# Kernel tuning notes

Measured on AMD Instinct MI355X. Metric: run time of the kernel, lower is better.

The kernel has to match this reference:

```python
import jax, jax.numpy as jnp
import numpy as np

DIM = 1024
DEPTH = 4
HEADS = 16
MLP_DIM = 4096
EPS = 1e-5


def layer_norm(x, g, b):
    mu = jnp.mean(x, axis=-1, keepdims=True)
    var = jnp.mean(jnp.square(x - mu), axis=-1, keepdims=True)
    return (x - mu) * jax.lax.rsqrt(var + EPS) * g + b


def setup_inputs() -> dict:
    key = jax.random.key(0)
    ks = jax.random.split(key, 8)
    s = DIM ** -0.5
    return {
        "x": jax.random.normal(ks[0], (2, 1024, DIM), dtype=jnp.float32),
        "ln1_g": jnp.ones((DIM,), jnp.float32),
        "ln1_b": jnp.zeros((DIM,), jnp.float32),
        "w_qkv": jax.random.normal(ks[1], (DIM, 3 * DIM), jnp.float32) * s,
        "w_o": jax.random.normal(ks[2], (DIM, DIM), jnp.float32) * s,
        "b_o": jnp.zeros((DIM,), jnp.float32),
        "ln2_g": jnp.ones((DIM,), jnp.float32),
        "ln2_b": jnp.zeros((DIM,), jnp.float32),
        "w1": jax.random.normal(ks[3], (DIM, MLP_DIM), jnp.float32) * s,
        "b1": jnp.zeros((MLP_DIM,), jnp.float32),
        "w2": jax.random.normal(ks[4], (MLP_DIM, DIM), jnp.float32) * (MLP_DIM ** -0.5),
        "b2": jnp.zeros((DIM,), jnp.float32),
    }


def reference(x, ln1_g, ln1_b, w_qkv, w_o, b_o, ln2_g, ln2_b, w1, b1, w2, b2):
    b, n, _ = x.shape
    h, d = HEADS, DIM // HEADS
    scale = DIM ** -0.5  # NB: full dim, as in source
    for _ in range(DEPTH):  # same (shared) weights each layer, per ModuleList([m]*depth)
        # --- attention with pre-norm + residual ---
        xn = layer_norm(x, ln1_g, ln1_b)
        qkv = xn @ w_qkv  # [b, n, 3*dim]
        qkv = qkv.reshape(b, n, 3, h, d)
        q = qkv[:, :, 0].transpose(0, 2, 1, 3)  # [b, h, n, d]
        k = qkv[:, :, 1].transpose(0, 2, 1, 3)
        v = qkv[:, :, 2].transpose(0, 2, 1, 3)
        scores = jnp.einsum('bhid,bhjd->bhij', q, k) * scale
        attn = jax.nn.softmax(scores, axis=-1)
        out = jnp.einsum('bhij,bhjd->bhid', attn, v)
        out = out.transpose(0, 2, 1, 3).reshape(b, n, DIM)
        x = out @ w_o + b_o + x
        # --- MLP with pre-norm + residual ---
        xn = layer_norm(x, ln2_g, ln2_b)
        hdn = jax.nn.gelu(xn @ w1 + b1, approximate=False)
        x = hdn @ w2 + b2 + x
    return x
```

## Files before the change

kernel.cpp:

```cpp
#include <hip/hip_runtime.h>
#include <math.h>

#define NTOK 2048
#define DIM_ 1024
#define NSEQ 1024
#define HEADS_ 16
#define HD 64
#define MLP_ 4096
#define EPS_ 1e-5f

#define FLAG_BIAS  1
#define FLAG_GELU  2
#define FLAG_QKV   8
#define FLAG_PART  16

typedef __attribute__((ext_vector_type(8))) short bf16x8;
typedef __attribute__((ext_vector_type(4))) float f32x4;

__device__ __forceinline__ unsigned short f2bf(float f) {
    unsigned u = __float_as_uint(f);
    u += 0x7fffu + ((u >> 16) & 1u);
    return (unsigned short)(u >> 16);
}
__device__ __forceinline__ float bf2f(unsigned short u) {
    return __uint_as_float(((unsigned)u) << 16);
}
__device__ __forceinline__ void gld16(const unsigned short* g, short* l) {
    __builtin_amdgcn_global_load_lds(
        (const __attribute__((address_space(1))) void*)g,
        (__attribute__((address_space(3))) void*)l, 16, 0, 0);
}
__device__ __forceinline__ float gelu_fast(float v) {
    float u = 1.5957691f * (v + 0.044715f * v * v * v);
    return v / (1.0f + __expf(-u));
}

__global__ __launch_bounds__(256) void wconv_kernel(const float* __restrict__ W,
                                                    unsigned short* __restrict__ Wt,
                                                    int K, int N,
                                                    float qscale, int qcols) {
    __shared__ float s[32][33];
    int n0 = blockIdx.x * 32, k0 = blockIdx.y * 32;
    int tx = threadIdx.x, ty = threadIdx.y;
    #pragma unroll
    for (int r = 0; r < 4; r++) {
        int k = ty + r * 8;
        s[k][tx] = W[(size_t)(k0 + k) * N + n0 + tx];
    }
    __syncthreads();
    #pragma unroll
    for (int r = 0; r < 4; r++) {
        int n = ty + r * 8;
        float v = s[tx][n];
        if (n0 + n < qcols) v *= qscale;
        Wt[(size_t)(n0 + n) * K + k0 + tx] = f2bf(v);
    }
}

__global__ __launch_bounds__(256) void ln_kernel(const float* __restrict__ src,
                                                 unsigned short* __restrict__ dst,
                                                 const float* __restrict__ g,
                                                 const float* __restrict__ b) {
    int row = blockIdx.x;
    int t = threadIdx.x;
    const float4* x4 = (const float4*)(src + (size_t)row * DIM_);
    float4 f = x4[t];
    float s  = f.x + f.y + f.z + f.w;
    float sq = f.x*f.x + f.y*f.y + f.z*f.z + f.w*f.w;
    __shared__ float ssum[256], ssq[256];
    ssum[t] = s; ssq[t] = sq;
    __syncthreads();
    for (int o = 128; o > 0; o >>= 1) {
        if (t < o) { ssum[t] += ssum[t+o]; ssq[t] += ssq[t+o]; }
        __syncthreads();
    }
    float mu  = ssum[0] * (1.0f / DIM_);
    float var = ssq[0] * (1.0f / DIM_) - mu * mu;
    float r = rsqrtf(var + EPS_);
    const float4* g4 = (const float4*)g;
    const float4* b4 = (const float4*)b;
    float4 gg = g4[t], bb = b4[t];
    ushort4 o4;
    o4.x = f2bf((f.x - mu) * r * gg.x + bb.x);
    o4.y = f2bf((f.y - mu) * r * gg.y + bb.y);
    o4.z = f2bf((f.z - mu) * r * gg.z + bb.z);
    o4.w = f2bf((f.w - mu) * r * gg.w + bb.w);
    ((ushort4*)(dst + (size_t)row * DIM_))[t] = o4;
}

__global__ __launch_bounds__(256) void gemm128_kernel(const unsigned short* __restrict__ A,
                                                      const unsigned short* __restrict__ Bt,
                                                      unsigned short* __restrict__ Cb,
                                                      unsigned short* __restrict__ Vt,
                                                      unsigned short* __restrict__ Ppart,
                                                      const float* __restrict__ bias,
                                                      int M, int N, int K, int KC,
                                                      int ldcb, int nx, int gz, int flags) {
    __shared__ short As[128 * 64];
    __shared__ short Bs[128 * 64];
    int id = blockIdx.x;
    int xcd = id & 7, s = id >> 3;
    int x = s % nx, pl = s / nx;
    int pair = pl * 8 + xcd;
    int z = pair % gz, y = pair / gz;
    int col0 = x * 128, row0 = y * 128;
    int k_beg = z * KC, k_end = k_beg + KC;

    int t = threadIdx.x;
    int lane = t & 63, w = t >> 6;
    int wm = w & 1, wn = w >> 1;

    f32x4 acc[4][4];
    #pragma unroll
    for (int mi = 0; mi < 4; mi++)
        #pragma unroll
        for (int ni = 0; ni < 4; ni++) acc[mi][ni] = (f32x4){0.f, 0.f, 0.f, 0.f};

    int r0 = t >> 3;
    int lchunk = ((t & 7) ^ (r0 & 7)) * 8;
    const unsigned short* Ag = A  + (size_t)(row0 + r0) * K + lchunk;
    const unsigned short* Bg = Bt + (size_t)(col0 + r0) * K + lchunk;
    short* Al = As + t * 8;
    short* Bl = Bs + t * 8;

    int m_l = lane & 15, quad = lane >> 4;
    int sw7 = m_l & 7;

    for (int k0 = k_beg; k0 < k_end; k0 += 64) {
        #pragma unroll
        for (int i = 0; i < 4; i++) {
            gld16(Ag + k0 + (size_t)i * 32 * K, Al + i * 2048);
            gld16(Bg + k0 + (size_t)i * 32 * K, Bl + i * 2048);
        }
        __syncthreads();

        #pragma unroll
        for (int kf = 0; kf < 2; kf++) {
            int cb = ((kf * 4 + quad) ^ sw7) * 8;
            bf16x8 af[4], bfr[4];
            #pragma unroll
            for (int mi = 0; mi < 4; mi++)
                af[mi]  = *(const bf16x8*)&As[(wm * 64 + mi * 16 + m_l) * 64 + cb];
            #pragma unroll
            for (int ni = 0; ni < 4; ni++)
                bfr[ni] = *(const bf16x8*)&Bs[(wn * 64 + ni * 16 + m_l) * 64 + cb];
            #pragma unroll
            for (int mi = 0; mi < 4; mi++)
                #pragma unroll
                for (int ni = 0; ni < 4; ni++)
                    acc[mi][ni] = __builtin_amdgcn_mfma_f32_16x16x32_bf16(af[mi], bfr[ni],
                                                                          acc[mi][ni], 0, 0, 0);
        }
        __syncthreads();
    }

    if (flags & FLAG_PART) {
        unsigned short* P = Ppart + (size_t)z * M * N;
        #pragma unroll
        for (int mi = 0; mi < 4; mi++)
            #pragma unroll
            for (int ni = 0; ni < 4; ni++) {
                int col = col0 + wn * 64 + ni * 16 + m_l;
                #pragma unroll
                for (int r = 0; r < 4; r++) {
                    int row = row0 + wm * 64 + mi * 16 + quad * 4 + r;
                    P[(size_t)row * N + col] = f2bf(acc[mi][ni][r]);
                }
            }
        return;
    }

    int colw = col0 + wn * 64;
    if ((flags & FLAG_QKV) && colw >= 2048) {
        int h = (colw - 2048) >> 6;
        #pragma unroll
        for (int mi = 0; mi < 4; mi++) {
            int tok0 = row0 + wm * 64 + mi * 16 + quad * 4;
            int bb = tok0 >> 10, nn = tok0 & 1023;
            #pragma unroll
            for (int ni = 0; ni < 4; ni++) {
                int d = ni * 16 + m_l;
                ushort4 o4;
                o4.x = f2bf(acc[mi][ni][0]);
                o4.y = f2bf(acc[mi][ni][1]);
                o4.z = f2bf(acc[mi][ni][2]);
                o4.w = f2bf(acc[mi][ni][3]);
                *(ushort4*)(Vt + ((size_t)(bb * 16 + h) * 64 + d) * 1024 + nn) = o4;
            }
        }
        return;
    }

    #pragma unroll
    for (int mi = 0; mi < 4; mi++)
        #pragma unroll
        for (int ni = 0; ni < 4; ni++) {
            int col = colw + ni * 16 + m_l;
            float bv = (flags & FLAG_BIAS) ? bias[col] : 0.0f;
            #pragma unroll
            for (int r = 0; r < 4; r++) {
                int row = row0 + wm * 64 + mi * 16 + quad * 4 + r;
                float v = acc[mi][ni][r] + bv;
                if (flags & FLAG_GELU) v = gelu_fast(v);
                Cb[(size_t)row * ldcb + col] = f2bf(v);
            }
        }
}

__global__ __launch_bounds__(256) void reduce_ln_kernel(const unsigned short* __restrict__ P,
                                                        int nsplit,
                                                        const float* __restrict__ bias,
                                                        const float* __restrict__ resid,
                                                        float* __restrict__ xc_out,
                                                        unsigned short* __restrict__ xn_out,
                                                        const float* __restrict__ g,
                                                        const float* __restrict__ b) {
    const int MN = NTOK * DIM_;
    int row = blockIdx.x;
    int t = threadIdx.x;
    size_t i = (size_t)row * DIM_ + t * 4;
    float4 y  = *(const float4*)(resid + i);
    float4 bi = *(const float4*)(bias + t * 4);
    y.x += bi.x; y.y += bi.y; y.z += bi.z; y.w += bi.w;
    for (int z = 0; z < nsplit; z++) {
        ushort4 p = *(const ushort4*)(P + (size_t)z * MN + i);
        y.x += bf2f(p.x); y.y += bf2f(p.y); y.z += bf2f(p.z); y.w += bf2f(p.w);
    }
    *(float4*)(xc_out + i) = y;
    if (!xn_out) return;

    float s  = y.x + y.y + y.z + y.w;
    float sq = y.x*y.x + y.y*y.y + y.z*y.z + y.w*y.w;
    __shared__ float ssum[256], ssq[256];
    ssum[t] = s; ssq[t] = sq;
    __syncthreads();
    for (int o = 128; o > 0; o >>= 1) {
        if (t < o) { ssum[t] += ssum[t+o]; ssq[t] += ssq[t+o]; }
        __syncthreads();
    }
    float mu  = ssum[0] * (1.0f / DIM_);
    float var = ssq[0] * (1.0f / DIM_) - mu * mu;
    float r = rsqrtf(var + EPS_);
    float4 gg = *(const float4*)(g + t * 4);
    float4 bb = *(const float4*)(b + t * 4);
    ushort4 o4;
    o4.x = f2bf((y.x - mu) * r * gg.x + bb.x);
    o4.y = f2bf((y.y - mu) * r * gg.y + bb.y);
    o4.z = f2bf((y.z - mu) * r * gg.z + bb.z);
    o4.w = f2bf((y.w - mu) * r * gg.w + bb.w);
    ((ushort4*)(xn_out + (size_t)row * DIM_))[t] = o4;
}

__global__ __launch_bounds__(512) void fattn_kernel(const unsigned short* __restrict__ qk,
                                                    const unsigned short* __restrict__ VtG,
                                                    unsigned short* __restrict__ out) {
    int idx = blockIdx.x;
    int qt = idx & 7;
    int h  = (idx >> 3) & 15;
    int b  = idx >> 7;
    int t  = threadIdx.x;
    int lane = t & 63, w = t >> 6;
    int m = lane & 15, quad = lane >> 4;

    __shared__ unsigned short Ks[64 * 64];
    __shared__ unsigned short Vs[64 * 64];
    __shared__ unsigned short Ps[8][16 * 72];

    const size_t base = (size_t)b * NSEQ * 2048;
    const int i0 = qt * 128 + w * 16;

    bf16x8 aq0, aq1;
    {
        const unsigned short* qrow = qk + base + (size_t)(i0 + m) * 2048 + h * HD;
        aq0 = *(const bf16x8*)(qrow + quad * 8);
        aq1 = *(const bf16x8*)(qrow + 32 + quad * 8);
    }

    f32x4 Oacc[4];
    #pragma unroll
    for (int dt = 0; dt < 4; dt++) Oacc[dt] = (f32x4){0.f, 0.f, 0.f, 0.f};
    float lsum[4] = {0.f, 0.f, 0.f, 0.f};

    int srow = t >> 3;
    int schunk = t & 7;
    int swc = schunk ^ (srow & 7);
    const unsigned short* Kg = qk + base + 1024 + h * HD + (size_t)srow * 2048 + schunk * 8;
    const unsigned short* Vg = VtG + ((size_t)(b * 16 + h) * 64 + srow) * 1024 + schunk * 8;
    unsigned short* Kl = &Ks[srow * 64 + swc * 8];
    unsigned short* Vl = &Vs[srow * 64 + swc * 8];

    for (int j0 = 0; j0 < NSEQ; j0 += 64) {
        *(bf16x8*)Kl = *(const bf16x8*)(Kg + (size_t)j0 * 2048);
        *(bf16x8*)Vl = *(const bf16x8*)(Vg + j0);
        __syncthreads();

        f32x4 s[4];
        #pragma unroll
        for (int nt = 0; nt < 4; nt++) {
            int jr = nt * 16 + m;
            const unsigned short* kr = &Ks[jr * 64];
            int x7 = jr & 7;
            bf16x8 b0 = *(const bf16x8*)(kr + (quad ^ x7) * 8);
            bf16x8 b1 = *(const bf16x8*)(kr + ((quad + 4) ^ x7) * 8);
            f32x4 a = (f32x4){0.f, 0.f, 0.f, 0.f};
            a = __builtin_amdgcn_mfma_f32_16x16x32_bf16(aq0, b0, a, 0, 0, 0);
            a = __builtin_amdgcn_mfma_f32_16x16x32_bf16(aq1, b1, a, 0, 0, 0);
            s[nt] = a;
        }

        #pragma unroll
        for (int r = 0; r < 4; r++) {
            float p0 = __expf(s[0][r]);
            float p1 = __expf(s[1][r]);
            float p2 = __expf(s[2][r]);
            float p3 = __expf(s[3][r]);
            lsum[r] += p0 + p1 + p2 + p3;
            unsigned short* pr = &Ps[w][(quad * 4 + r) * 72 + m];
            pr[0]  = f2bf(p0);
            pr[16] = f2bf(p1);
            pr[32] = f2bf(p2);
            pr[48] = f2bf(p3);
        }

        const unsigned short* pa = &Ps[w][m * 72 + quad * 8];
        bf16x8 ap0 = *(const bf16x8*)pa;
        bf16x8 ap1 = *(const bf16x8*)(pa + 32);
        #pragma unroll
        for (int dt = 0; dt < 4; dt++) {
            int dr = dt * 16 + m;
            const unsigned short* vr = &Vs[dr * 64];
            int x7 = dr & 7;
            bf16x8 b0 = *(const bf16x8*)(vr + (quad ^ x7) * 8);
            bf16x8 b1 = *(const bf16x8*)(vr + ((quad + 4) ^ x7) * 8);
            Oacc[dt] = __builtin_amdgcn_mfma_f32_16x16x32_bf16(ap0, b0, Oacc[dt], 0, 0, 0);
            Oacc[dt] = __builtin_amdgcn_mfma_f32_16x16x32_bf16(ap1, b1, Oacc[dt], 0, 0, 0);
        }
        __syncthreads();
    }

    #pragma unroll
    for (int r = 0; r < 4; r++) {
        float rs = lsum[r];
        rs += __shfl_xor(rs, 1);
        rs += __shfl_xor(rs, 2);
        rs += __shfl_xor(rs, 4);
        rs += __shfl_xor(rs, 8);
        lsum[r] = rs;
    }

    #pragma unroll
    for (int r = 0; r < 4; r++) {
        float inv = 1.0f / lsum[r];
        int row = i0 + quad * 4 + r;
        unsigned short* orow = out + ((size_t)(b * NSEQ + row)) * DIM_ + h * HD + m;
        orow[0]  = f2bf(Oacc[0][r] * inv);
        orow[16] = f2bf(Oacc[1][r] * inv);
        orow[32] = f2bf(Oacc[2][r] * inv);
        orow[48] = f2bf(Oacc[3][r] * inv);
    }
}

extern "C" void kernel_launch(void* const* d_in, const int* in_sizes, int n_in,
                              void* d_out, int out_size, void* d_ws, size_t ws_size,
                              hipStream_t stream) {
    const float* x    = (const float*)d_in[0];
    const float* ln1g = (const float*)d_in[1];
    const float* ln1b = (const float*)d_in[2];
    const float* wqkv = (const float*)d_in[3];
    const float* wo   = (const float*)d_in[4];
    const float* bo   = (const float*)d_in[5];
    const float* ln2g = (const float*)d_in[6];
    const float* ln2b = (const float*)d_in[7];
    const float* w1   = (const float*)d_in[8];
    const float* b1   = (const float*)d_in[9];
    const float* w2   = (const float*)d_in[10];
    const float* b2   = (const float*)d_in[11];
    float* out = (float*)d_out;

    char* ws = (char*)d_ws;
    float*          xcur = (float*)(ws);
    unsigned short* aout = (unsigned short*)(ws + (8u<<20));
    unsigned short* xn   = (unsigned short*)(ws + (12u<<20));
    unsigned short* qk   = (unsigned short*)(ws + (16u<<20));
    unsigned short* VtG  = (unsigned short*)(ws + (24u<<20));
    unsigned short* hdn  = (unsigned short*)(ws + (28u<<20));
    unsigned short* wtqkv= (unsigned short*)(ws + (44u<<20));
    unsigned short* wto  = (unsigned short*)(ws + (50u<<20));
    unsigned short* wt1  = (unsigned short*)(ws + (52u<<20));
    unsigned short* wt2  = (unsigned short*)(ws + (60u<<20));
    unsigned short* opart  = (unsigned short*)(ws + (12u<<20));
    unsigned short* m2part = (unsigned short*)(ws + (8u<<20));

    wconv_kernel<<<dim3(3*DIM_/32, DIM_/32), dim3(32,8), 0, stream>>>(wqkv, wtqkv, DIM_, 3*DIM_,
                                                                      0.03125f, DIM_);
    wconv_kernel<<<dim3(DIM_/32,   DIM_/32), dim3(32,8), 0, stream>>>(wo,   wto, DIM_, DIM_, 1.f, 0);
    wconv_kernel<<<dim3(MLP_/32,   DIM_/32), dim3(32,8), 0, stream>>>(w1,   wt1, DIM_, MLP_, 1.f, 0);
    wconv_kernel<<<dim3(DIM_/32,   MLP_/32), dim3(32,8), 0, stream>>>(w2,   wt2, MLP_, DIM_, 1.f, 0);

    for (int layer = 0; layer < 4; layer++) {
        if (layer == 0)
            ln_kernel<<<NTOK, 256, 0, stream>>>(x, xn, ln1g, ln1b);
        gemm128_kernel<<<384, 256, 0, stream>>>(
            xn, wtqkv, qk, VtG, nullptr, nullptr,
            NTOK, 3*DIM_, DIM_, DIM_, 2048, 24, 1, FLAG_QKV);
        fattn_kernel<<<256, 512, 0, stream>>>(qk, VtG, aout);
        gemm128_kernel<<<512, 256, 0, stream>>>(
            aout, wto, nullptr, nullptr, opart, nullptr,
            NTOK, DIM_, DIM_, DIM_/4, 0, 8, 4, FLAG_PART);
        reduce_ln_kernel<<<NTOK, 256, 0, stream>>>(
            opart, 4, bo, (layer == 0 ? x : xcur), xcur, xn, ln2g, ln2b);
        gemm128_kernel<<<512, 256, 0, stream>>>(
            xn, wt1, hdn, nullptr, nullptr, b1,
            NTOK, MLP_, DIM_, DIM_, MLP_, 32, 1, FLAG_BIAS | FLAG_GELU);
        gemm128_kernel<<<512, 256, 0, stream>>>(
            hdn, wt2, nullptr, nullptr, m2part, nullptr,
            NTOK, DIM_, MLP_, MLP_/4, 0, 8, 4, FLAG_PART);
        if (layer < 3)
            reduce_ln_kernel<<<NTOK, 256, 0, stream>>>(
                m2part, 4, b2, xcur, xcur, xn, ln1g, ln1b);
        else
            reduce_ln_kernel<<<NTOK, 256, 0, stream>>>(
                m2part, 4, b2, xcur, out, nullptr, nullptr, nullptr);
    }
}
```

Baseline: 650.9 us.

## Switch GEMMs to 256x256 tiles with double-buffered LDS and MFMA priority

Replaces the 128x128 single-buffered GEMM with a 256x256-tile, 512-thread kernel. It double-buffers LDS so global loads for tile k+2 overlap compute, and raises wave priority around the MFMA bursts. The goal is more data reuse per tile and hidden load latency. The MLP down-projection moves to an 8-way split-K with a relocated partial buffer. The cost is fewer blocks (96-256 on a 256-CU part, so under-occupancy), 128 KB of LDS per block, and extra barriers and reduction traffic.

After: 831.0 us. 1.28x slower.

```diff
diff --git a/kernel.cpp b/kernel.cpp
--- a/kernel.cpp
+++ b/kernel.cpp
@@ -88,82 +88,105 @@
     ((ushort4*)(dst + (size_t)row * DIM_))[t] = o4;
 }
 
-__global__ __launch_bounds__(256) void gemm128_kernel(const unsigned short* __restrict__ A,
-                                                      const unsigned short* __restrict__ Bt,
-                                                      unsigned short* __restrict__ Cb,
-                                                      unsigned short* __restrict__ Vt,
-                                                      unsigned short* __restrict__ Ppart,
-                                                      const float* __restrict__ bias,
-                                                      int M, int N, int K, int KC,
-                                                      int ldcb, int nx, int gz, int flags) {
-    __shared__ short As[128 * 64];
-    __shared__ short Bs[128 * 64];
+__global__ __launch_bounds__(512, 2) void gemm256_kernel(const unsigned short* __restrict__ A,
+                                                         const unsigned short* __restrict__ Bt,
+                                                         unsigned short* __restrict__ Cb,
+                                                         unsigned short* __restrict__ Vt,
+                                                         unsigned short* __restrict__ Ppart,
+                                                         const float* __restrict__ bias,
+                                                         int M, int N, int K, int KC,
+                                                         int ldcb, int nx, int gz, int flags) {
+    __shared__ short As[2][256 * 64];
+    __shared__ short Bs[2][256 * 64];
+    const int BUFS = 256 * 64;
+
     int id = blockIdx.x;
     int xcd = id & 7, s = id >> 3;
     int x = s % nx, pl = s / nx;
     int pair = pl * 8 + xcd;
     int z = pair % gz, y = pair / gz;
-    int col0 = x * 128, row0 = y * 128;
-    int k_beg = z * KC, k_end = k_beg + KC;
+    int col0 = x * 256, row0 = y * 256;
+    int k_beg = z * KC;
+    int nt = KC >> 6;
 
     int t = threadIdx.x;
     int lane = t & 63, w = t >> 6;
     int wm = w & 1, wn = w >> 1;
-
-    f32x4 acc[4][4];
-    #pragma unroll
-    for (int mi = 0; mi < 4; mi++)
+    int m_l = lane & 15, quad = lane >> 4;
+    int sw7 = m_l & 7;
+
+    f32x4 acc[8][4];
+    #pragma unroll
+    for (int mi = 0; mi < 8; mi++)
         #pragma unroll
         for (int ni = 0; ni < 4; ni++) acc[mi][ni] = (f32x4){0.f, 0.f, 0.f, 0.f};
 
     int r0 = t >> 3;
     int lchunk = ((t & 7) ^ (r0 & 7)) * 8;
-    const unsigned short* Ag = A  + (size_t)(row0 + r0) * K + lchunk;
-    const unsigned short* Bg = Bt + (size_t)(col0 + r0) * K + lchunk;
-    short* Al = As + t * 8;
-    short* Bl = Bs + t * 8;
-
-    int m_l = lane & 15, quad = lane >> 4;
-    int sw7 = m_l & 7;
-
-    for (int k0 = k_beg; k0 < k_end; k0 += 64) {
+    const unsigned short* Ag = A  + (size_t)(row0 + r0) * K + k_beg + lchunk;
+    const unsigned short* Bg = Bt + (size_t)(col0 + r0) * K + k_beg + lchunk;
+    short* Al = &As[0][t * 8];
+    short* Bl = &Bs[0][t * 8];
+
+    auto stage = [&](int buf_, int tt_) {
         #pragma unroll
         for (int i = 0; i < 4; i++) {
-            gld16(Ag + k0 + (size_t)i * 32 * K, Al + i * 2048);
-            gld16(Bg + k0 + (size_t)i * 32 * K, Bl + i * 2048);
-        }
-        __syncthreads();
+            gld16(Ag + tt_ * 64 + (size_t)i * 64 * K, Al + buf_ * BUFS + i * 4096);
+            gld16(Bg + tt_ * 64 + (size_t)i * 64 * K, Bl + buf_ * BUFS + i * 4096);
+        }
+    };
+    stage(0, 0);
+    stage(1, 1);
+
+    for (int tt = 0; tt < nt; tt++) {
+        int cur = tt & 1;
+        if (tt == nt - 1) asm volatile("s_waitcnt vmcnt(0)" ::: "memory");
+        else              asm volatile("s_waitcnt vmcnt(8)" ::: "memory");
+        __builtin_amdgcn_s_barrier();
+        asm volatile("" ::: "memory");
+        const short* Ab = &As[cur][0];
+        const short* Bb = &Bs[cur][0];
 
         #pragma unroll
         for (int kf = 0; kf < 2; kf++) {
             int cb = ((kf * 4 + quad) ^ sw7) * 8;
-            bf16x8 af[4], bfr[4];
-            #pragma unroll
-            for (int mi = 0; mi < 4; mi++)
-                af[mi]  = *(const bf16x8*)&As[(wm * 64 + mi * 16 + m_l) * 64 + cb];
+            bf16x8 bfr[4];
             #pragma unroll
             for (int ni = 0; ni < 4; ni++)
-                bfr[ni] = *(const bf16x8*)&Bs[(wn * 64 + ni * 16 + m_l) * 64 + cb];
+                bfr[ni] = *(const bf16x8*)&Bb[(wn * 64 + ni * 16 + m_l) * 64 + cb];
             #pragma unroll
-            for (int mi = 0; mi < 4; mi++)
+            for (int half = 0; half < 2; half++) {
+                bf16x8 af[4];
                 #pragma unroll
-                for (int ni = 0; ni < 4; ni++)
-                    acc[mi][ni] = __builtin_amdgcn_mfma_f32_16x16x32_bf16(af[mi], bfr[ni],
-                                                                          acc[mi][ni], 0, 0, 0);
-        }
-        __syncthreads();
+                for (int mi = 0; mi < 4; mi++)
+                    af[mi] = *(const bf16x8*)&Ab[(wm * 128 + (half * 4 + mi) * 16 + m_l) * 64 + cb];
+                __builtin_amdgcn_s_barrier();
+                asm volatile("" ::: "memory");
+                __builtin_amdgcn_s_setprio(1);
+                #pragma unroll
+                for (int mi = 0; mi < 4; mi++)
+                    #pragma unroll
+                    for (int ni = 0; ni < 4; ni++)
+                        acc[half * 4 + mi][ni] = __builtin_amdgcn_mfma_f32_16x16x32_bf16(
+                            af[mi], bfr[ni], acc[half * 4 + mi][ni], 0, 0, 0);
+                __builtin_amdgcn_s_setprio(0);
+                __builtin_amdgcn_s_barrier();
+                asm volatile("" ::: "memory");
+            }
+        }
+        if (tt + 2 < nt) stage(cur, tt + 2);
     }
 
     if (flags & FLAG_PART) {
         unsigned short* P = Ppart + (size_t)z * M * N;
         #pragma unroll
-        for (int mi = 0; mi < 4; mi++)
+        for (int mi = 0; mi < 8; mi++)
             #pragma unroll
             for (int ni = 0; ni < 4; ni++) {
                 int col = col0 + wn * 64 + ni * 16 + m_l;
                 #pragma unroll
                 for (int r = 0; r < 4; r++) {
-                    int row = row0 + wm * 64 + mi * 16 + quad * 4 + r;
+                    int row = row0 + wm * 128 + mi * 16 + quad * 4 + r;
                     P[(size_t)row * N + col] = f2bf(acc[mi][ni][r]);
                 }
             }
@@ -174,8 +197,8 @@
     if ((flags & FLAG_QKV) && colw >= 2048) {
         int h = (colw - 2048) >> 6;
         #pragma unroll
-        for (int mi = 0; mi < 4; mi++) {
-            int tok0 = row0 + wm * 64 + mi * 16 + quad * 4;
+        for (int mi = 0; mi < 8; mi++) {
+            int tok0 = row0 + wm * 128 + mi * 16 + quad * 4;
             int bb = tok0 >> 10, nn = tok0 & 1023;
             #pragma unroll
             for (int ni = 0; ni < 4; ni++) {
@@ -192,14 +215,14 @@
     }
 
     #pragma unroll
-    for (int mi = 0; mi < 4; mi++)
+    for (int mi = 0; mi < 8; mi++)
         #pragma unroll
         for (int ni = 0; ni < 4; ni++) {
             int col = colw + ni * 16 + m_l;
             float bv = (flags & FLAG_BIAS) ? bias[col] : 0.0f;
             #pragma unroll
             for (int r = 0; r < 4; r++) {
-                int row = row0 + wm * 64 + mi * 16 + quad * 4 + r;
+                int row = row0 + wm * 128 + mi * 16 + quad * 4 + r;
                 float v = acc[mi][ni][r] + bv;
                 if (flags & FLAG_GELU) v = gelu_fast(v);
                 Cb[(size_t)row * ldcb + col] = f2bf(v);
@@ -389,7 +412,7 @@
     unsigned short* wt1  = (unsigned short*)(ws + (52u<<20));
     unsigned short* wt2  = (unsigned short*)(ws + (60u<<20));
     unsigned short* opart  = (unsigned short*)(ws + (12u<<20));
-    unsigned short* m2part = (unsigned short*)(ws + (8u<<20));
+    unsigned short* m2part = (unsigned short*)(ws + (68u<<20));
 
     wconv_kernel<<<dim3(3*DIM_/32, DIM_/32), dim3(32,8), 0, stream>>>(wqkv, wtqkv, DIM_, 3*DIM_,
                                                                       0.03125f, DIM_);
@@ -400,26 +423,26 @@
     for (int layer = 0; layer < 4; layer++) {
         if (layer == 0)
             ln_kernel<<<NTOK, 256, 0, stream>>>(x, xn, ln1g, ln1b);
-        gemm128_kernel<<<384, 256, 0, stream>>>(
+        gemm256_kernel<<<96, 512, 0, stream>>>(
             xn, wtqkv, qk, VtG, nullptr, nullptr,
-            NTOK, 3*DIM_, DIM_, DIM_, 2048, 24, 1, FLAG_QKV);
+            NTOK, 3*DIM_, DIM_, DIM_, 2048, 12, 1, FLAG_QKV);
         fattn_kernel<<<256, 512, 0, stream>>>(qk, VtG, aout);
-        gemm128_kernel<<<512, 256, 0, stream>>>(
+        gemm256_kernel<<<128, 512, 0, stream>>>(
             aout, wto, nullptr, nullptr, opart, nullptr,
-            NTOK, DIM_, DIM_, DIM_/4, 0, 8, 4, FLAG_PART);
+            NTOK, DIM_, DIM_, DIM_/4, 0, 4, 4, FLAG_PART);
         reduce_ln_kernel<<<NTOK, 256, 0, stream>>>(
             opart, 4, bo, (layer == 0 ? x : xcur), xcur, xn, ln2g, ln2b);
-        gemm128_kernel<<<512, 256, 0, stream>>>(
+        gemm256_kernel<<<128, 512, 0, stream>>>(
             xn, wt1, hdn, nullptr, nullptr, b1,
-            NTOK, MLP_, DIM_, DIM_, MLP_, 32, 1, FLAG_BIAS | FLAG_GELU);
-        gemm128_kernel<<<512, 256, 0, stream>>>(
+            NTOK, MLP_, DIM_, DIM_, MLP_, 16, 1, FLAG_BIAS | FLAG_GELU);
+        gemm256_kernel<<<256, 512, 0, stream>>>(
             hdn, wt2, nullptr, nullptr, m2part, nullptr,
-            NTOK, DIM_, MLP_, MLP_/4, 0, 8, 4, FLAG_PART);
+            NTOK, DIM_, MLP_, MLP_/8, 0, 4, 8, FLAG_PART);
         if (layer < 3)
             reduce_ln_kernel<<<NTOK, 256, 0, stream>>>(
-                m2part, 4, b2, xcur, xcur, xn, ln1g, ln1b);
+                m2part, 8, b2, xcur, xcur, xn, ln1g, ln1b);
         else
             reduce_ln_kernel<<<NTOK, 256, 0, stream>>>(
-                m2part, 4, b2, xcur, out, nullptr, nullptr, nullptr);
-    }
-}
+                m2part, 8, b2, xcur, out, nullptr, nullptr, nullptr);
+    }
+}
```

## Double-buffer K/V tiles in attention with register prefetch and reorder block mapping

Applied to the files above, without the earlier changes.

The flash-attention kernel now prefetches the next K/V tile into registers while the current tile is computed. It double-buffers the shared-memory tiles so the trailing barrier per iteration can be dropped. The block index mapping is also changed so consecutive blocks cover different heads and batches instead of different query tiles of one head. This hides global-load latency and halves the barriers, at the cost of more shared memory and register pressure. It also changes L2 locality for K/V reuse across query tiles.

New measurement: 629.2 us. -3.3%, faster.

```diff
diff --git a/kernel.cpp b/kernel.cpp
--- a/kernel.cpp
+++ b/kernel.cpp
@@ -255,15 +255,15 @@
                                                     const unsigned short* __restrict__ VtG,
                                                     unsigned short* __restrict__ out) {
     int idx = blockIdx.x;
-    int qt = idx & 7;
-    int h  = (idx >> 3) & 15;
-    int b  = idx >> 7;
+    int qt = idx >> 5;
+    int h  = idx & 15;
+    int b  = (idx >> 4) & 1;
     int t  = threadIdx.x;
     int lane = t & 63, w = t >> 6;
     int m = lane & 15, quad = lane >> 4;
 
-    __shared__ unsigned short Ks[64 * 64];
-    __shared__ unsigned short Vs[64 * 64];
+    __shared__ unsigned short Ks[2][64 * 64];
+    __shared__ unsigned short Vs[2][64 * 64];
     __shared__ unsigned short Ps[8][16 * 72];
 
     const size_t base = (size_t)b * NSEQ * 2048;
@@ -286,19 +286,26 @@
     int swc = schunk ^ (srow & 7);
     const unsigned short* Kg = qk + base + 1024 + h * HD + (size_t)srow * 2048 + schunk * 8;
     const unsigned short* Vg = VtG + ((size_t)(b * 16 + h) * 64 + srow) * 1024 + schunk * 8;
-    unsigned short* Kl = &Ks[srow * 64 + swc * 8];
-    unsigned short* Vl = &Vs[srow * 64 + swc * 8];
-
-    for (int j0 = 0; j0 < NSEQ; j0 += 64) {
-        *(bf16x8*)Kl = *(const bf16x8*)(Kg + (size_t)j0 * 2048);
-        *(bf16x8*)Vl = *(const bf16x8*)(Vg + j0);
+    const int sloff = srow * 64 + swc * 8;
+
+    bf16x8 kreg = *(const bf16x8*)(Kg);
+    bf16x8 vreg = *(const bf16x8*)(Vg);
+
+    for (int jt = 0; jt < NSEQ / 64; jt++) {
+        int cur = jt & 1;
+        *(bf16x8*)&Ks[cur][sloff] = kreg;
+        *(bf16x8*)&Vs[cur][sloff] = vreg;
         __syncthreads();
+        if (jt + 1 < NSEQ / 64) {
+            kreg = *(const bf16x8*)(Kg + (size_t)(jt + 1) * 64 * 2048);
+            vreg = *(const bf16x8*)(Vg + (jt + 1) * 64);
+        }
 
         f32x4 s[4];
         #pragma unroll
         for (int nt = 0; nt < 4; nt++) {
             int jr = nt * 16 + m;
-            const unsigned short* kr = &Ks[jr * 64];
+            const unsigned short* kr = &Ks[cur][jr * 64];
             int x7 = jr & 7;
             bf16x8 b0 = *(const bf16x8*)(kr + (quad ^ x7) * 8);
             bf16x8 b1 = *(const bf16x8*)(kr + ((quad + 4) ^ x7) * 8);
@@ -328,14 +335,13 @@
         #pragma unroll
         for (int dt = 0; dt < 4; dt++) {
             int dr = dt * 16 + m;
-            const unsigned short* vr = &Vs[dr * 64];
+            const unsigned short* vr = &Vs[cur][dr * 64];
             int x7 = dr & 7;
             bf16x8 b0 = *(const bf16x8*)(vr + (quad ^ x7) * 8);
             bf16x8 b1 = *(const bf16x8*)(vr + ((quad + 4) ^ x7) * 8);
             Oacc[dt] = __builtin_amdgcn_mfma_f32_16x16x32_bf16(ap0, b0, Oacc[dt], 0, 0, 0);
             Oacc[dt] = __builtin_amdgcn_mfma_f32_16x16x32_bf16(ap1, b1, Oacc[dt], 0, 0, 0);
         }
-        __syncthreads();
     }
 
     #pragma unroll
```
